# Kernel tuning notes

Hardware: AMD Instinct MI355X
Metric: run time of the kernel (lower is better)

## Reference

```python
import jax, jax.numpy as jnp
import numpy as np


def _rule_stack(x_q):
    # x_q: [B, 2, 4]; a/b are the two context panels, per attribute column -> [B, 4]
    a = x_q[:, 0, :]
    b = x_q[:, 1, :]
    # 13 fixed rules applied elementwise across the 4 attribute columns -> [B, 4, 13]
    return jnp.stack([
        a,
        b - 2.0, b - 1.0, b + 1.0, b + 2.0,
        a - b, a + b,
        jnp.minimum(a, b), jnp.maximum(a, b),
        b + 2.0, b + 1.0, b - 2.0, b - 1.0,
    ], axis=-1)


def setup_inputs() -> dict:
    key = jax.random.key(0)
    k1, k2, k3, k4 = jax.random.split(key, 4)
    B, Z = 262144, 512
    z = jax.random.normal(k1, (B, Z), dtype=jnp.float32)
    x_q = jax.random.normal(k2, (B, 2, 4), dtype=jnp.float32)
    # rule_encoder: Linear(z_dim -> 4*13)
    W = jax.random.normal(k3, (Z, 52), dtype=jnp.float32) / np.sqrt(Z)
    b = jax.random.normal(k4, (52,), dtype=jnp.float32) * 0.01
    return {"z": z, "x_q": x_q, "W": W, "b": b}


def reference(z, x_q, W, b):
    logits = (z @ W + b).reshape(-1, 4, 13)          # [B, 4, 13]
    rule_probs = jax.nn.softmax(logits, axis=-1)       # [B, 4, 13]
    rules = _rule_stack(x_q)                           # [B, 4, 13]
    y_q = jnp.sum(rules * rule_probs, axis=-1)         # [B, 4]
    return y_q[:, None, :]                             # [B, 1, 4]
```

## Files before the change

### kernel.cpp

```cpp
#include <hip/hip_runtime.h>
#include <stdint.h>

typedef __bf16 bf16_t;
typedef bf16_t bf16x8 __attribute__((ext_vector_type(8)));
typedef float f32x2 __attribute__((ext_vector_type(2)));
typedef float f32x4 __attribute__((ext_vector_type(4)));
typedef uint32_t u32x4 __attribute__((ext_vector_type(4)));
typedef uint16_t u16x8 __attribute__((ext_vector_type(8)));

union FragU { u32x4 u; bf16x8 v; u16x8 s; };

__device__ __forceinline__ uint16_t f2bf_rne(float f) {
  uint32_t u = __float_as_uint(f);
  return (uint16_t)((u + 0x7fffu + ((u >> 16) & 1u)) >> 16);
}

__global__ __launch_bounds__(256) void pack_w_kernel(
    const float* __restrict__ W, u32x4* __restrict__ wf) {
  int idx = blockIdx.x * 256 + threadIdx.x;
  if (idx >= 4096) return;
  int lane = idx & 63;
  int nt   = (idx >> 6) & 3;
  int ks   = idx >> 8;
  int n  = nt * 16 + (lane & 15);
  int kb = ks * 32 + (lane >> 4) * 8;
  FragU hi;
#pragma unroll
  for (int j = 0; j < 8; ++j) {
    float w = (n < 52) ? W[(kb + j) * 52 + n] : 0.0f;
    hi.s[j] = f2bf_rne(w);
  }
  wf[idx] = hi.u;
}

#define MFMA16(a, b, c) __builtin_amdgcn_mfma_f32_16x16x32_bf16((a), (b), (c), 0, 0, 0)

__global__ __launch_bounds__(256, 4) void raven_main_kernel(
    const float* __restrict__ z, const float* __restrict__ xq,
    const u32x4* __restrict__ wfh,
    const float* __restrict__ bias, float* __restrict__ out) {
  __shared__ __align__(16) unsigned char smem[33792];
  __shared__ float lds_bias[52];

  const int tid  = threadIdx.x;
  const int wave = tid >> 6;
  const int lane = tid & 63;
  const int r  = lane & 15;
  const int kg = lane >> 4;

  if (tid < 52) lds_bias[tid] = bias[tid];

  const long long brow = (long long)blockIdx.x * 128;
  const long long wrow = brow + (long long)wave * 32;
  const float* zb = z + wrow * 512;

  unsigned char* stg = smem + wave * 8192;

  const int rloc = lane >> 3;
  const int foff = 4 * ((lane & 7) ^ rloc);

  f32x4 acc[2][4];
#pragma unroll
  for (int mt = 0; mt < 2; ++mt)
#pragma unroll
    for (int nt = 0; nt < 4; ++nt) {
      f32x4 zv = {0.0f, 0.0f, 0.0f, 0.0f};
      acc[mt][nt] = zv;
    }

#define STAGE_CHUNK(ks_, buf_)                                                  \
  {                                                                             \
    const float* g_ = zb + rloc * 512 + (ks_) * 32 + foff;                      \
    _Pragma("unroll")                                                           \
    for (int i_ = 0; i_ < 4; ++i_)                                              \
      __builtin_amdgcn_global_load_lds(                                         \
          (const __attribute__((address_space(1))) void*)(g_ + i_ * 8 * 512),   \
          (__attribute__((address_space(3))) void*)((buf_) + i_ * 1024),        \
          16, 0, 0);                                                            \
  }

#define LOADB(ks_, set_)                                                        \
  {                                                                             \
    const u32x4* ph_ = wfh + (ks_) * 256 + lane;                                \
    _Pragma("unroll")                                                           \
    for (int nt_ = 0; nt_ < 4; ++nt_) {                                         \
      bh[set_][nt_].u = ph_[nt_ * 64];                                          \
    }                                                                           \
  }

  FragU bh[2][4];

  LOADB(0, 0);
  STAGE_CHUNK(0, stg);
  LOADB(1, 1);
  STAGE_CHUNK(1, stg + 4096);

  const int swz = (r & 7) << 4;

#pragma unroll
  for (int ks = 0; ks < 16; ++ks) {
    unsigned char* cur = stg + (ks & 1) * 4096;

    if (ks < 15) asm volatile("s_waitcnt vmcnt(8)" ::: "memory");
    else         asm volatile("s_waitcnt vmcnt(0)" ::: "memory");
    __builtin_amdgcn_sched_barrier(0);

    const unsigned char* c0 = cur + r * 128;
    const unsigned char* c1 = cur + (r + 16) * 128;
    f32x4 a00 = *(const f32x4*)(c0 + ((kg * 32) ^ swz));
    f32x4 a01 = *(const f32x4*)(c0 + ((kg * 32 + 16) ^ swz));
    f32x4 a10 = *(const f32x4*)(c1 + ((kg * 32) ^ swz));
    f32x4 a11 = *(const f32x4*)(c1 + ((kg * 32 + 16) ^ swz));

    FragU h0, h1;
#pragma unroll
    for (int j = 0; j < 4; ++j) {
      h0.v[j]     = (bf16_t)a00[j];
      h0.v[4 + j] = (bf16_t)a01[j];
      h1.v[j]     = (bf16_t)a10[j];
      h1.v[4 + j] = (bf16_t)a11[j];
    }

    const int cs = ks & 1;
#pragma unroll
    for (int nt = 0; nt < 4; ++nt) {
      acc[0][nt] = MFMA16(h0.v, bh[cs][nt].v, acc[0][nt]);
      acc[1][nt] = MFMA16(h1.v, bh[cs][nt].v, acc[1][nt]);
    }
    __builtin_amdgcn_sched_barrier(0);

    if (ks < 14) {
      LOADB(ks + 2, cs);
      STAGE_CHUNK(ks + 2, cur);
    }
  }
#undef STAGE_CHUNK
#undef LOADB

  __syncthreads();

  float (*lds_t)[132] = (float(*)[132])smem;
#pragma unroll
  for (int mt = 0; mt < 2; ++mt)
#pragma unroll
    for (int nt = 0; nt < 4; ++nt)
      *(f32x4*)&lds_t[nt * 16 + r][wave * 32 + mt * 16 + kg * 4] = acc[mt][nt];

  __syncthreads();

  {
    const int row = tid >> 1;
    const int gp  = (tid & 1) * 2;
    const long long grow = brow + row;
    f32x2 res;
#pragma unroll
    for (int gi = 0; gi < 2; ++gi) {
      const int g = gp + gi;
      float a  = xq[grow * 8 + g];
      float bq = xq[grow * 8 + 4 + g];
      float l[13];
      float m = -1e30f;
#pragma unroll
      for (int u = 0; u < 13; ++u) {
        l[u] = lds_t[g * 13 + u][row] + lds_bias[g * 13 + u];
        m = fmaxf(m, l[u]);
      }
      float s = 0.0f;
#pragma unroll
      for (int u = 0; u < 13; ++u) {
        float e = __expf(l[u] - m);
        l[u] = e;
        s += e;
      }
      float num = a * l[0]
                + (bq - 2.0f) * (l[1] + l[11])
                + (bq - 1.0f) * (l[2] + l[12])
                + (bq + 1.0f) * (l[3] + l[10])
                + (bq + 2.0f) * (l[4] + l[9])
                + (a - bq) * l[5]
                + (a + bq) * l[6]
                + fminf(a, bq) * l[7]
                + fmaxf(a, bq) * l[8];
      res[gi] = num / s;
    }
    *(f32x2*)(out + grow * 4 + gp) = res;
  }
}

extern "C" void kernel_launch(void* const* d_in, const int* in_sizes, int n_in,
                              void* d_out, int out_size, void* d_ws, size_t ws_size,
                              hipStream_t stream) {
  const float* z    = (const float*)d_in[0];
  const float* xq   = (const float*)d_in[1];
  const float* W    = (const float*)d_in[2];
  const float* bias = (const float*)d_in[3];
  float* out = (float*)d_out;

  const int B = in_sizes[0] / 512;

  u32x4* wf = (u32x4*)d_ws;

  hipLaunchKernelGGL(pack_w_kernel, dim3(16), dim3(256), 0, stream, W, wf);

  const int blocks = B / 128;
  hipLaunchKernelGGL(raven_main_kernel, dim3(blocks), dim3(256), 0, stream,
                     z, xq, (const u32x4*)wf, bias, out);
}
```

Measured before the change: 108.1 us.

## Double K-chunk size per pipeline stage to deepen in-flight loads

Each pipeline stage now stages 64 K-columns of z per wave instead of 32, halving the number of loop iterations and doubling the bytes in flight per wait. The LDS staging buffer grows to 64 KB and launch bounds drop from 4 to 2 blocks per CU to fit. The aim is to amortize waitcnt and loop overhead and keep more memory requests outstanding in this bandwidth-bound kernel. The cost is lower occupancy and more registers for the doubled B fragments.

```diff
diff --git a/kernel.cpp b/kernel.cpp
--- a/kernel.cpp
+++ b/kernel.cpp
@@ -35,11 +35,11 @@
 
 #define MFMA16(a, b, c) __builtin_amdgcn_mfma_f32_16x16x32_bf16((a), (b), (c), 0, 0, 0)
 
-__global__ __launch_bounds__(256, 4) void raven_main_kernel(
+__global__ __launch_bounds__(256, 2) void raven_main_kernel(
     const float* __restrict__ z, const float* __restrict__ xq,
     const u32x4* __restrict__ wfh,
     const float* __restrict__ bias, float* __restrict__ out) {
-  __shared__ __align__(16) unsigned char smem[33792];
+  __shared__ __align__(16) unsigned char smem[65536];
   __shared__ float lds_bias[52];
 
   const int tid  = threadIdx.x;
@@ -54,10 +54,10 @@
   const long long wrow = brow + (long long)wave * 32;
   const float* zb = z + wrow * 512;
 
-  unsigned char* stg = smem + wave * 8192;
-
-  const int rloc = lane >> 3;
-  const int foff = 4 * ((lane & 7) ^ rloc);
+  unsigned char* stg = smem + wave * 16384;
+
+  const int rloc4 = lane >> 4;
+  const int slot  = lane & 15;
 
   f32x4 acc[2][4];
 #pragma unroll
@@ -70,66 +70,72 @@
 
 #define STAGE_CHUNK(ks_, buf_)                                                  \
   {                                                                             \
-    const float* g_ = zb + rloc * 512 + (ks_) * 32 + foff;                      \
     _Pragma("unroll")                                                           \
-    for (int i_ = 0; i_ < 4; ++i_)                                              \
+    for (int i_ = 0; i_ < 8; ++i_) {                                            \
+      const int srow_ = i_ * 4 + rloc4;                                         \
+      const int foff_ = 4 * (slot ^ (srow_ & 7));                               \
+      const float* g_ = zb + srow_ * 512 + (ks_) * 64 + foff_;                  \
       __builtin_amdgcn_global_load_lds(                                         \
-          (const __attribute__((address_space(1))) void*)(g_ + i_ * 8 * 512),   \
+          (const __attribute__((address_space(1))) void*)g_,                    \
           (__attribute__((address_space(3))) void*)((buf_) + i_ * 1024),        \
           16, 0, 0);                                                            \
+    }                                                                           \
   }
 
 #define LOADB(ks_, set_)                                                        \
   {                                                                             \
-    const u32x4* ph_ = wfh + (ks_) * 256 + lane;                                \
+    const u32x4* p0_ = wfh + (2 * (ks_)) * 256 + lane;                          \
+    const u32x4* p1_ = wfh + (2 * (ks_) + 1) * 256 + lane;                      \
     _Pragma("unroll")                                                           \
     for (int nt_ = 0; nt_ < 4; ++nt_) {                                         \
-      bh[set_][nt_].u = ph_[nt_ * 64];                                          \
+      bh[set_][nt_].u     = p0_[nt_ * 64];                                      \
+      bh[set_][4 + nt_].u = p1_[nt_ * 64];                                      \
     }                                                                           \
   }
 
-  FragU bh[2][4];
+  FragU bh[2][8];
 
   LOADB(0, 0);
   STAGE_CHUNK(0, stg);
   LOADB(1, 1);
-  STAGE_CHUNK(1, stg + 4096);
+  STAGE_CHUNK(1, stg + 8192);
 
   const int swz = (r & 7) << 4;
 
 #pragma unroll
-  for (int ks = 0; ks < 16; ++ks) {
-    unsigned char* cur = stg + (ks & 1) * 4096;
-
-    if (ks < 15) asm volatile("s_waitcnt vmcnt(8)" ::: "memory");
-    else         asm volatile("s_waitcnt vmcnt(0)" ::: "memory");
+  for (int ks = 0; ks < 8; ++ks) {
+    unsigned char* cur = stg + (ks & 1) * 8192;
+
+    if (ks < 7) asm volatile("s_waitcnt vmcnt(16)" ::: "memory");
+    else        asm volatile("s_waitcnt vmcnt(0)"  ::: "memory");
     __builtin_amdgcn_sched_barrier(0);
 
-    const unsigned char* c0 = cur + r * 128;
-    const unsigned char* c1 = cur + (r + 16) * 128;
-    f32x4 a00 = *(const f32x4*)(c0 + ((kg * 32) ^ swz));
-    f32x4 a01 = *(const f32x4*)(c0 + ((kg * 32 + 16) ^ swz));
-    f32x4 a10 = *(const f32x4*)(c1 + ((kg * 32) ^ swz));
-    f32x4 a11 = *(const f32x4*)(c1 + ((kg * 32 + 16) ^ swz));
-
-    FragU h0, h1;
-#pragma unroll
-    for (int j = 0; j < 4; ++j) {
-      h0.v[j]     = (bf16_t)a00[j];
-      h0.v[4 + j] = (bf16_t)a01[j];
-      h1.v[j]     = (bf16_t)a10[j];
-      h1.v[4 + j] = (bf16_t)a11[j];
-    }
+    FragU h[2][2];
+#pragma unroll
+    for (int c = 0; c < 2; ++c)
+#pragma unroll
+      for (int mt = 0; mt < 2; ++mt) {
+        const unsigned char* cm = cur + (mt * 16 + r) * 256;
+        f32x4 a0 = *(const f32x4*)(cm + ((c * 128 + kg * 32) ^ swz));
+        f32x4 a1 = *(const f32x4*)(cm + ((c * 128 + kg * 32 + 16) ^ swz));
+#pragma unroll
+        for (int j = 0; j < 4; ++j) {
+          h[c][mt].v[j]     = (bf16_t)a0[j];
+          h[c][mt].v[4 + j] = (bf16_t)a1[j];
+        }
+      }
 
     const int cs = ks & 1;
 #pragma unroll
-    for (int nt = 0; nt < 4; ++nt) {
-      acc[0][nt] = MFMA16(h0.v, bh[cs][nt].v, acc[0][nt]);
-      acc[1][nt] = MFMA16(h1.v, bh[cs][nt].v, acc[1][nt]);
-    }
+    for (int c = 0; c < 2; ++c)
+#pragma unroll
+      for (int nt = 0; nt < 4; ++nt) {
+        acc[0][nt] = MFMA16(h[c][0].v, bh[cs][c * 4 + nt].v, acc[0][nt]);
+        acc[1][nt] = MFMA16(h[c][1].v, bh[cs][c * 4 + nt].v, acc[1][nt]);
+      }
     __builtin_amdgcn_sched_barrier(0);
 
-    if (ks < 14) {
+    if (ks < 6) {
       LOADB(ks + 2, cs);
       STAGE_CHUNK(ks + 2, cur);
     }
```

Measured after the change: 106.0 us, median of 2. 2.0% less time.
